# Performance work log

Measured on AMD Instinct MI355X. Metric: run time of the kernel, lower is better.

The kernel has to match this reference:

```python
import jax, jax.numpy as jnp
import numpy as np
import math

B, S, T = 32, 128, 64
FEAT = 16
H = 1024
V = 32000


def _gru_step(x, h, wih, whh, bih, bhh):
    # torch nn.GRU cell: gates ordered (r, z, n)
    gi = x @ wih.T + bih
    gh = h @ whh.T + bhh
    ir, iz, in_ = jnp.split(gi, 3, axis=-1)
    hr, hz, hn = jnp.split(gh, 3, axis=-1)
    r = jax.nn.sigmoid(ir + hr)
    z = jax.nn.sigmoid(iz + hz)
    n = jnp.tanh(in_ + r * hn)
    return (1.0 - z) * n + z * h


def _forward(features, target_tokens, temp_W, temp_b, hum_W, hum_b, cloud_W, cloud_b,
             time_W, time_b, other_W, other_b, fi_W, fi_b,
             enc_wih, enc_whh, enc_bih, enc_bhh, emb, attn_W, attn_b,
             dec_wih, dec_whh, dec_bih, dec_bhh, out_W, out_b):
    b = features.shape[0]
    # per-feature projections (dropout = identity in eval mode)
    temp = features[:, :, 0:1] @ temp_W.T + temp_b
    hum = features[:, :, 1:2] @ hum_W.T + hum_b
    cloud = features[:, :, 2:3] @ cloud_W.T + cloud_b
    time = features[:, :, -5:-3] @ time_W.T + time_b
    other_in = jnp.concatenate([features[:, :, 3:-5], features[:, :, -3:]], axis=2)
    other = other_in @ other_W.T + other_b
    concat = jnp.concatenate([temp, hum, cloud, time, other], axis=2)  # [B,S,2H]
    proj = jnp.tanh(concat @ fi_W.T + fi_b)  # [B,S,H]

    # encoder GRU over time
    def enc_step(h, x):
        h2 = _gru_step(x, h, enc_wih, enc_whh, enc_bih, enc_bhh)
        return h2, h2
    h0 = jnp.zeros((b, H), proj.dtype)
    h_last, enc_outs = jax.lax.scan(enc_step, h0, proj.transpose(1, 0, 2))
    enc_out = enc_outs.transpose(1, 0, 2)  # [B,S,H]

    # attention keys computed once (loop-invariant in the original)
    keys = enc_out @ attn_W.T + attn_b  # [B,S,H]
    scale = 1.0 / math.sqrt(H)

    # decoder: teacher_forcing_ratio = 1.0 -> input at step t is target_tokens[:, t-1]
    def dec_step(h, tok):
        e = emb[tok]  # [B,H]
        scores = jnp.einsum('bh,bsh->bs', h, keys) * scale
        w = jax.nn.softmax(scores, axis=-1)
        ctx = jnp.einsum('bs,bsh->bh', w, enc_out)
        x = jnp.concatenate([e, ctx], axis=-1)  # [B,2H]
        h2 = _gru_step(x, h, dec_wih, dec_whh, dec_bih, dec_bhh)
        pred = jnp.concatenate([h2, ctx], axis=-1) @ out_W.T + out_b  # [B,V]
        return h2, pred

    _, preds = jax.lax.scan(dec_step, h_last, target_tokens[:, :-1].T)  # [T-1,B,V]
    outputs = jnp.zeros((b, target_tokens.shape[1], V), preds.dtype)
    outputs = outputs.at[:, 0, target_tokens[0, 0]].set(1.0)
    outputs = outputs.at[:, 1:, :].set(preds.transpose(1, 0, 2))
    return outputs


def setup_inputs() -> dict:
    key = jax.random.key(0)
    ks = jax.random.split(key, 32)
    nrm = lambda k, sh: jax.random.normal(k, sh, jnp.float32) * 0.05
    Hq = H // 4
    d = {}
    d['features'] = jax.random.normal(ks[0], (B, S, FEAT), jnp.float32)
    d['target_tokens'] = jax.random.randint(ks[1], (B, T), 0, V, dtype=jnp.int32)
    d['temp_W'] = nrm(ks[2], (Hq, 1)); d['temp_b'] = nrm(ks[3], (Hq,))
    d['hum_W'] = nrm(ks[4], (Hq, 1)); d['hum_b'] = nrm(ks[5], (Hq,))
    d['cloud_W'] = nrm(ks[6], (Hq, 1)); d['cloud_b'] = nrm(ks[7], (Hq,))
    d['time_W'] = nrm(ks[8], (Hq, 2)); d['time_b'] = nrm(ks[9], (Hq,))
    d['other_W'] = nrm(ks[10], (H, FEAT - 5)); d['other_b'] = nrm(ks[11], (H,))
    d['fi_W'] = nrm(ks[12], (H, 2 * H)); d['fi_b'] = nrm(ks[13], (H,))
    d['enc_wih'] = nrm(ks[14], (3 * H, H)); d['enc_whh'] = nrm(ks[15], (3 * H, H))
    d['enc_bih'] = nrm(ks[16], (3 * H,)); d['enc_bhh'] = nrm(ks[17], (3 * H,))
    d['emb'] = nrm(ks[18], (V, H))
    d['attn_W'] = nrm(ks[19], (H, H)); d['attn_b'] = nrm(ks[20], (H,))
    d['dec_wih'] = nrm(ks[21], (3 * H, 2 * H)); d['dec_whh'] = nrm(ks[22], (3 * H, H))
    d['dec_bih'] = nrm(ks[23], (3 * H,)); d['dec_bhh'] = nrm(ks[24], (3 * H,))
    d['out_W'] = nrm(ks[25], (V, 2 * H)); d['out_b'] = nrm(ks[26], (V,))
    return d


def reference(features, target_tokens, temp_W, temp_b, hum_W, hum_b, cloud_W, cloud_b,
              time_W, time_b, other_W, other_b, fi_W, fi_b,
              enc_wih, enc_whh, enc_bih, enc_bhh, emb, attn_W, attn_b,
              dec_wih, dec_whh, dec_bih, dec_bhh, out_W, out_b):
    return _forward(features, target_tokens, temp_W, temp_b, hum_W, hum_b, cloud_W, cloud_b,
                    time_W, time_b, other_W, other_b, fi_W, fi_b,
                    enc_wih, enc_whh, enc_bih, enc_bhh, emb, attn_W, attn_b,
                    dec_wih, dec_whh, dec_bih, dec_bhh, out_W, out_b)
```

## Files before the change

### kernel.cpp

```cpp
#include <hip/hip_runtime.h>

typedef float f32x4 __attribute__((ext_vector_type(4)));
typedef __bf16 bf16x8 __attribute__((ext_vector_type(8)));

#define DI static __device__ __forceinline__

DI unsigned short f2bf(float f) {
  unsigned u = __float_as_uint(f);
  u = (u + 0x7fffu + ((u >> 16) & 1u)) >> 16;
  return (unsigned short)u;
}
DI unsigned pk2(float lo, float hi) {
  return (unsigned)f2bf(lo) | ((unsigned)f2bf(hi) << 16);
}
DI float bflo(unsigned u) { return __uint_as_float(u << 16); }
DI float bfhi(unsigned u) { return __uint_as_float(u & 0xffff0000u); }
DI float sigm(float x) { return 1.0f / (1.0f + expf(-x)); }

DI void gl_lds16(const unsigned short* g, unsigned short* l) {
  __builtin_amdgcn_global_load_lds(
      (const __attribute__((address_space(1))) unsigned int*)g,
      (__attribute__((address_space(3))) unsigned int*)l, 16, 0, 0);
}

DI void st32_sc1(unsigned* p, unsigned v) {
  __hip_atomic_store(p, v, __ATOMIC_RELAXED, __HIP_MEMORY_SCOPE_AGENT);
}
DI void st64_sc1(unsigned long long* p, unsigned long long v) {
  __hip_atomic_store(p, v, __ATOMIC_RELAXED, __HIP_MEMORY_SCOPE_AGENT);
}
DI int ldw(const int* p) {
  return __hip_atomic_load(p, __ATOMIC_RELAXED, __HIP_MEMORY_SCOPE_AGENT);
}
DI void stw(int* p, int v) {
  __hip_atomic_store(p, v, __ATOMIC_RELAXED, __HIP_MEMORY_SCOPE_AGENT);
}
DI void waitword(const int* w, int gen) {
  while (ldw(w) < gen) __builtin_amdgcn_s_sleep(1);
  asm volatile("" ::: "memory");
}

__global__ void k_fold(const float* __restrict__ tW, const float* __restrict__ tb,
                       const float* __restrict__ hW, const float* __restrict__ hb,
                       const float* __restrict__ cW, const float* __restrict__ cb,
                       const float* __restrict__ tiW, const float* __restrict__ tib,
                       const float* __restrict__ oW, const float* __restrict__ ob,
                       const float* __restrict__ fiW, const float* __restrict__ fib,
                       float* __restrict__ M, float* __restrict__ b0v)
{
  int g = blockIdx.x * 256 + threadIdx.x;
  if (g >= 1024 * 17) return;
  int h = g / 17, f = g - h * 17;
  const float* fw = fiW + (size_t)h * 2048;
  float s = 0.f;
  if (f == 16) {
    for (int k = 0; k < 256; ++k) s += fw[k] * tb[k];
    for (int k = 0; k < 256; ++k) s += fw[256 + k] * hb[k];
    for (int k = 0; k < 256; ++k) s += fw[512 + k] * cb[k];
    for (int k = 0; k < 256; ++k) s += fw[768 + k] * tib[k];
    for (int r = 0; r < 1024; ++r) s += fw[1024 + r] * ob[r];
    b0v[h] = s + fib[h];
  } else if (f == 0) {
    for (int k = 0; k < 256; ++k) s += fw[k] * tW[k];
    M[h * 16 + 0] = s;
  } else if (f == 1) {
    for (int k = 0; k < 256; ++k) s += fw[256 + k] * hW[k];
    M[h * 16 + 1] = s;
  } else if (f == 2) {
    for (int k = 0; k < 256; ++k) s += fw[512 + k] * cW[k];
    M[h * 16 + 2] = s;
  } else if (f == 11) {
    for (int k = 0; k < 256; ++k) s += fw[768 + k] * tiW[2 * k];
    M[h * 16 + 11] = s;
  } else if (f == 12) {
    for (int k = 0; k < 256; ++k) s += fw[768 + k] * tiW[2 * k + 1];
    M[h * 16 + 12] = s;
  } else {
    int col = (f <= 10) ? (f - 3) : (f - 5);
    for (int r = 0; r < 1024; ++r) s += fw[1024 + r] * oW[r * 11 + col];
    M[h * 16 + f] = s;
  }
}

__global__ __launch_bounds__(256)
void k_proj(const float* __restrict__ feat, const float* __restrict__ M,
            const float* __restrict__ b0v, unsigned short* __restrict__ proj)
{
  __shared__ float ft[16];
  int bs = blockIdx.x;
  int h = blockIdx.y * 256 + threadIdx.x;
  if (threadIdx.x < 16) ft[threadIdx.x] = feat[bs * 16 + threadIdx.x];
  __syncthreads();
  float sum = b0v[h];
  const float* mr = M + h * 16;
#pragma unroll
  for (int f = 0; f < 16; ++f) sum += mr[f] * ft[f];
  proj[(size_t)bs * 1024 + h] = f2bf(tanhf(sum));
}

__global__ void k_conv(const float* __restrict__ s, unsigned short* __restrict__ d, int n8)
{
  for (long i = (long)blockIdx.x * 256 + threadIdx.x; i < n8; i += (long)gridDim.x * 256) {
    const float* p = s + i * 8;
    f32x4 a = *(const f32x4*)p, b = *(const f32x4*)(p + 4);
    uint4 o;
    o.x = pk2(a[0], a[1]); o.y = pk2(a[2], a[3]);
    o.z = pk2(b[0], b[1]); o.w = pk2(b[2], b[3]);
    *(uint4*)(d + i * 8) = o;
  }
}

__global__ void k_conv_str(const float* __restrict__ s, unsigned short* __restrict__ d)
{
  int r = blockIdx.x;
  int c = threadIdx.x * 4;
  f32x4 a = *(const f32x4*)(s + (size_t)r * 2048 + c);
  uint2 o; o.x = pk2(a[0], a[1]); o.y = pk2(a[2], a[3]);
  *(uint2*)(d + (size_t)r * 1024 + c) = o;
}

__global__ void k_gather_e(const int* __restrict__ toks, const float* __restrict__ emb,
                           unsigned short* __restrict__ e_bf)
{
  int row = blockIdx.x;
  int t = row >> 5, b = row & 31;
  unsigned short* dst = e_bf + (size_t)row * 1024 + threadIdx.x * 4;
  if (t < 63) {
    int tok = toks[b * 64 + t];
    f32x4 a = *(const f32x4*)(emb + (size_t)tok * 1024 + threadIdx.x * 4);
    uint2 o; o.x = pk2(a[0], a[1]); o.y = pk2(a[2], a[3]);
    *(uint2*)dst = o;
  } else {
    uint2 o; o.x = 0u; o.y = 0u;
    *(uint2*)dst = o;
  }
}

__global__ void k_onehot(const int* __restrict__ toks, float* __restrict__ out)
{
  int i = blockIdx.x * 256 + threadIdx.x;
  if (i >= 32 * 32000) return;
  int b = i / 32000, v = i - b * 32000;
  out[(size_t)b * 64 * 32000 + v] = (v == toks[0]) ? 1.0f : 0.0f;
}

template<int MODE>
__global__ __launch_bounds__(256)
void gemm_bf(const unsigned short* __restrict__ A, const unsigned short* __restrict__ B,
             const float* __restrict__ bias, float* __restrict__ Cf,
             unsigned short* __restrict__ Cb,
             int tiles_m, int K, int lda, int ldb, int ldc, int coloff)
{
  __shared__ unsigned short As[4096];
  __shared__ unsigned short Bs[4096];
  const int nblk = gridDim.x;
  const int cpx = nblk >> 3;
  const int bid = blockIdx.x;
  const int id = (bid & 7) * cpx + (bid >> 3);
  const int tm = id % tiles_m, tn = id / tiles_m;
  const int tid = threadIdx.x;
  const int lane = tid & 63, wave = tid >> 6;
  const int wm = (wave & 1) << 6, wn = (wave >> 1) << 6;
  const int r0 = tid >> 2, kc0 = (tid & 3) << 3;
  const unsigned short* ga0 = A + (size_t)(tm * 128 + r0) * lda + kc0;
  const unsigned short* ga1 = A + (size_t)(tm * 128 + 64 + r0) * lda + kc0;
  const unsigned short* gb0 = B + (size_t)(tn * 128 + r0) * ldb + kc0;
  const unsigned short* gb1 = B + (size_t)(tn * 128 + 64 + r0) * ldb + kc0;
  const int lr = lane & 15, lkb = (lane >> 4) << 3;

  f32x4 acc[4][4];
#pragma unroll
  for (int m = 0; m < 4; ++m)
#pragma unroll
    for (int n = 0; n < 4; ++n) { acc[m][n][0]=0.f; acc[m][n][1]=0.f; acc[m][n][2]=0.f; acc[m][n][3]=0.f; }

  for (int kt = 0; kt < K; kt += 32) {
    __syncthreads();
    gl_lds16(ga0 + kt, &As[tid * 8]);
    gl_lds16(ga1 + kt, &As[(tid + 256) * 8]);
    gl_lds16(gb0 + kt, &Bs[tid * 8]);
    gl_lds16(gb1 + kt, &Bs[(tid + 256) * 8]);
    __syncthreads();
    bf16x8 af[4], bfv[4];
#pragma unroll
    for (int m = 0; m < 4; ++m) af[m] = *(const bf16x8*)&As[(wm + m * 16 + lr) * 32 + lkb];
#pragma unroll
    for (int n = 0; n < 4; ++n) bfv[n] = *(const bf16x8*)&Bs[(wn + n * 16 + lr) * 32 + lkb];
#pragma unroll
    for (int m = 0; m < 4; ++m)
#pragma unroll
      for (int n = 0; n < 4; ++n)
        acc[m][n] = __builtin_amdgcn_mfma_f32_16x16x32_bf16(af[m], bfv[n], acc[m][n], 0, 0, 0);
  }

#pragma unroll
  for (int m = 0; m < 4; ++m) {
    int rb = tm * 128 + wm + m * 16 + ((lane >> 4) << 2);
#pragma unroll
    for (int n = 0; n < 4; ++n) {
      int c = tn * 128 + wn + n * 16 + lr;
      float bb = bias[c];
#pragma unroll
      for (int i = 0; i < 4; ++i) {
        float v = acc[m][n][i] + bb;
        int r = rb + i;
        if (MODE == 0) {
          Cf[(size_t)r * ldc + c] = v;
        } else if (MODE == 1) {
          Cb[(size_t)r * ldc + c] = f2bf(v);
        } else {
          if (r < 2016) {
            int t = r >> 5, b2 = r & 31;
            Cf[((size_t)b2 * 64 + t + 1) * 32000 + coloff + c] = v;
          }
        }
      }
    }
  }
}

__global__ __launch_bounds__(256, 1)
void k_enc_scan(const float* __restrict__ gi_all, const float* __restrict__ whh,
                const float* __restrict__ bhh, float* __restrict__ hfp,
                unsigned short* __restrict__ enc_bf,
                int* __restrict__ arrE, int* __restrict__ relE)
{
  const int tid = threadIdx.x;
  const int blk = blockIdx.x;
  if (blk == 64) {
    if (tid < 64) {
      for (int g = 1; g <= 128; ++g) {
        for (;;) {
          int v = ldw(&arrE[tid << 2]);
          if (__all(v >= g)) break;
          __builtin_amdgcn_s_sleep(1);
        }
        asm volatile("" ::: "memory");
        if (tid == 0) stw(relE, g);
      }
    }
    return;
  }

  __shared__ unsigned short W[48 * 1024];
  __shared__ float Cred[4 * 2 * 3 * 64 * 4];
  const int lane = tid & 63, wave = tid >> 6;
  const int j0 = blk * 16;

  for (int i = tid; i < 48 * 128; i += 256) {
    int r = i >> 7, c = i & 127;
    int gr = ((r >> 4) << 10) + j0 + (r & 15);
    const float* src = whh + ((size_t)gr << 10) + (c << 3);
    f32x4 a = *(const f32x4*)src, b = *(const f32x4*)(src + 4);
    uint4 o;
    o.x = pk2(a[0], a[1]); o.y = pk2(a[2], a[3]);
    o.z = pk2(b[0], b[1]); o.w = pk2(b[2], b[3]);
    *(uint4*)&W[(r << 10) + ((c ^ (r & 7)) << 3)] = o;
  }
  __syncthreads();

  int cb[2], cj[2], clb[2], creg[2], cm[2];
  float bh0[2], bh1[2], bh2[2];
  float hp[2] = {0.f, 0.f};
#pragma unroll
  for (int cc = 0; cc < 2; ++cc) {
    int cell = tid + (cc << 8);
    cb[cc] = cell >> 4; cj[cc] = cell & 15;
    clb[cc] = ((cb[cc] & 15) >> 2) * 16;
    creg[cc] = cb[cc] & 3; cm[cc] = cb[cc] >> 4;
    bh0[cc] = bhh[j0 + cj[cc]];
    bh1[cc] = bhh[1024 + j0 + cj[cc]];
    bh2[cc] = bhh[2048 + j0 + cj[cc]];
  }

#pragma unroll 1
  for (int s = 0; s < 128; ++s) {
    float gp[2][3];
#pragma unroll
    for (int cc = 0; cc < 2; ++cc) {
      const float* gi = gi_all + ((size_t)cb[cc] * 128 + s) * 3072 + j0 + cj[cc];
      gp[cc][0] = gi[0]; gp[cc][1] = gi[1024]; gp[cc][2] = gi[2048];
    }

    f32x4 acc[2][3];
#pragma unroll
    for (int m = 0; m < 2; ++m)
#pragma unroll
      for (int n = 0; n < 3; ++n) { acc[m][n][0]=0.f; acc[m][n][1]=0.f; acc[m][n][2]=0.f; acc[m][n][3]=0.f; }

    if (s > 0) {
      waitword(relE, s);
      const unsigned short* hr = enc_bf + (size_t)(s - 1) * 1024;
      const int k0 = wave << 8;
      bf16x8 af[2][8];
#pragma unroll
      for (int kk = 0; kk < 8; ++kk) {
        int k = k0 + kk * 32 + ((lane >> 4) << 3);
        af[0][kk] = *(const bf16x8*)(hr + (size_t)(lane & 15) * 131072 + k);
        af[1][kk] = *(const bf16x8*)(hr + (size_t)(16 + (lane & 15)) * 131072 + k);
      }
#pragma unroll
      for (int kk = 0; kk < 8; ++kk) {
        int c = ((k0 + kk * 32) >> 3) + (lane >> 4);
#pragma unroll
        for (int n = 0; n < 3; ++n) {
          int wr = n * 16 + (lane & 15);
          bf16x8 bfr = *(const bf16x8*)&W[(wr << 10) + ((c ^ (wr & 7)) << 3)];
          acc[0][n] = __builtin_amdgcn_mfma_f32_16x16x32_bf16(af[0][kk], bfr, acc[0][n], 0, 0, 0);
          acc[1][n] = __builtin_amdgcn_mfma_f32_16x16x32_bf16(af[1][kk], bfr, acc[1][n], 0, 0, 0);
        }
      }
    }
#pragma unroll
    for (int m = 0; m < 2; ++m)
#pragma unroll
      for (int n = 0; n < 3; ++n)
        *(f32x4*)&Cred[((((wave * 2 + m) * 3 + n) * 64) + lane) << 2] = acc[m][n];
    __syncthreads();

    float h2v[2];
#pragma unroll
    for (int cc = 0; cc < 2; ++cc) {
      int lj = clb[cc] + cj[cc], reg = creg[cc], m = cm[cc];
      float Cr = 0.f, Cz = 0.f, Cn = 0.f;
#pragma unroll
      for (int w = 0; w < 4; ++w) {
        Cr += Cred[((((w * 2 + m) * 3 + 0) * 64 + lj) << 2) + reg];
        Cz += Cred[((((w * 2 + m) * 3 + 1) * 64 + lj) << 2) + reg];
        Cn += Cred[((((w * 2 + m) * 3 + 2) * 64 + lj) << 2) + reg];
      }
      float r = sigm(gp[cc][0] + Cr + bh0[cc]);
      float z = sigm(gp[cc][1] + Cz + bh1[cc]);
      float n = tanhf(gp[cc][2] + r * (Cn + bh2[cc]));
      float h2 = (1.f - z) * n + z * hp[cc];
      h2v[cc] = h2; hp[cc] = h2;
    }
    if (s == 127) {
      hfp[cb[0] * 1024 + j0 + cj[0]] = h2v[0];
      hfp[cb[1] * 1024 + j0 + cj[1]] = h2v[1];
    }
    unsigned short s0 = f2bf(h2v[0]), s1 = f2bf(h2v[1]);
    unsigned o0 = (unsigned)__shfl_xor((int)(unsigned)s0, 1);
    unsigned o1 = (unsigned)__shfl_xor((int)(unsigned)s1, 1);
    if ((tid & 1) == 0) {
      int j = cj[0];
      st32_sc1((unsigned*)&enc_bf[((size_t)cb[0] * 128 + s) * 1024 + j0 + j],
               (unsigned)s0 | (o0 << 16));
      st32_sc1((unsigned*)&enc_bf[((size_t)cb[1] * 128 + s) * 1024 + j0 + j],
               (unsigned)s1 | (o1 << 16));
    }
    __syncthreads();
    if (tid == 0) stw(&arrE[blk << 2], s + 1);
  }
}

__global__ __launch_bounds__(256, 1)
void k_dec_scan(const float* __restrict__ gi_e, const float* __restrict__ whh,
                const float* __restrict__ wih, const float* __restrict__ bhh,
                const unsigned short* __restrict__ keys,
                const unsigned short* __restrict__ enc_bf,
                unsigned short* __restrict__ hcat, const float* __restrict__ hfp0,
                int* __restrict__ arrC, int* __restrict__ relC,
                int* __restrict__ arrH, int* __restrict__ relH)
{
  const int tid = threadIdx.x;
  const int blk = blockIdx.x;
  if (blk == 128) {
    if (tid < 64) {
      for (int g = 1; g <= 63; ++g) {
        for (;;) {
          int v = (tid < 32) ? ldw(&arrC[tid << 2]) : g;
          if (__all(v >= g)) break;
          __builtin_amdgcn_s_sleep(1);
        }
        asm volatile("" ::: "memory");
        if (tid == 0) stw(relC, g);
        for (;;) {
          int v0 = ldw(&arrH[(tid * 2) << 2]);
          int v1 = ldw(&arrH[(tid * 2 + 1) << 2]);
          if (__all(v0 >= g && v1 >= g)) break;
          __builtin_amdgcn_s_sleep(1);
        }
        asm volatile("" ::: "memory");
        if (tid == 0) stw(relH, g);
      }
    }
    return;
  }

  __shared__ unsigned short Wh[32 * 1024];
  __shared__ unsigned short Wx[32 * 1024];
  __shared__ float Cred[4 * 2 * 2 * 64 * 4];
  __shared__ unsigned short hsh[1024];
  __shared__ float sarr[128];
  __shared__ float earr[128];
  const int lane = tid & 63, wave = tid >> 6;
  const int j0 = blk * 8;

  for (int i = tid; i < 32 * 128; i += 256) {
    int r = i >> 7, c = i & 127;
    int off = (r << 10) + ((c ^ (r & 7)) << 3);
    uint4 oh, ox;
    oh.x = oh.y = oh.z = oh.w = 0u; ox = oh;
    if (r < 24) {
      int gr = ((r >> 3) << 10) + j0 + (r & 7);
      const float* sh = whh + ((size_t)gr << 10) + (c << 3);
      f32x4 a = *(const f32x4*)sh, b = *(const f32x4*)(sh + 4);
      oh.x = pk2(a[0], a[1]); oh.y = pk2(a[2], a[3]);
      oh.z = pk2(b[0], b[1]); oh.w = pk2(b[2], b[3]);
      const float* sx = wih + ((size_t)gr << 11) + 1024 + (c << 3);
      f32x4 e = *(const f32x4*)sx, f = *(const f32x4*)(sx + 4);
      ox.x = pk2(e[0], e[1]); ox.y = pk2(e[2], e[3]);
      ox.z = pk2(f[0], f[1]); ox.w = pk2(f[2], f[3]);
    }
    *(uint4*)&Wh[off] = oh;
    *(uint4*)&Wx[off] = ox;
  }
  __syncthreads();

  const int gb = tid >> 3, gj = tid & 7;
  const int glb = ((gb & 15) >> 2) * 16;
  const int greg = gb & 3, gm = gb >> 4;
  const float bh0 = bhh[j0 + gj];
  const float bh1 = bhh[1024 + j0 + gj];
  const float bh2 = bhh[2048 + j0 + gj];
  float hpv = hfp0[gb * 1024 + j0 + gj];

#pragma unroll 1
  for (int t = 0; t < 63; ++t) {
    const int gen = t + 1;
    const float* gie = gi_e + ((size_t)t * 32 + gb) * 3072 + j0 + gj;
    float g0 = gie[0], g1 = gie[1024], g2 = gie[2048];

    if (blk < 32) {
      if (t) waitword(relH, t);
      const int b = blk;
      const unsigned short* hsrc = (t == 0)
          ? (enc_bf + (size_t)b * 131072 + (size_t)127 * 1024)
          : (hcat + ((size_t)(t - 1) * 32 + b) * 2048);
      *(uint2*)&hsh[tid * 4] = *(const uint2*)(hsrc + tid * 4);
      __syncthreads();
      {
        int sp = tid >> 1, kh = (tid & 1) << 9;
        const unsigned short* kr = keys + ((size_t)b * 128 + sp) * 1024 + kh;
        float a = 0.f;
#pragma unroll 8
        for (int c = 0; c < 512; c += 8) {
          uint4 kv = *(const uint4*)(kr + c);
          uint4 hv = *(const uint4*)&hsh[kh + c];
          a += bflo(kv.x) * bflo(hv.x) + bfhi(kv.x) * bfhi(hv.x)
             + bflo(kv.y) * bflo(hv.y) + bfhi(kv.y) * bfhi(hv.y)
             + bflo(kv.z) * bflo(hv.z) + bfhi(kv.z) * bfhi(hv.z)
             + bflo(kv.w) * bflo(hv.w) + bfhi(kv.w) * bfhi(hv.w);
        }
        a += __shfl_xor(a, 1);
        if ((tid & 1) == 0) sarr[sp] = a * 0.03125f;
      }
      __syncthreads();
      float mx = -1e30f;
#pragma unroll 16
      for (int i2 = 0; i2 < 128; ++i2) mx = fmaxf(mx, sarr[i2]);
      if (tid < 128) earr[tid] = expf(sarr[tid] - mx);
      __syncthreads();
      float sum = 0.f;
#pragma unroll 16
      for (int i2 = 0; i2 < 128; ++i2) sum += earr[i2];
      float winv = 1.f / sum;
      f32x4 cacc; cacc[0]=0.f; cacc[1]=0.f; cacc[2]=0.f; cacc[3]=0.f;
      const unsigned short* eb = enc_bf + ((size_t)b << 17) + tid * 4;
#pragma unroll 4
      for (int s2 = 0; s2 < 128; ++s2) {
        float w = earr[s2] * winv;
        uint2 ev = *(const uint2*)(eb + ((size_t)s2 << 10));
        cacc[0] += w * bflo(ev.x); cacc[1] += w * bfhi(ev.x);
        cacc[2] += w * bflo(ev.y); cacc[3] += w * bfhi(ev.y);
      }
      unsigned long long cw = (unsigned long long)pk2(cacc[0], cacc[1])
                            | ((unsigned long long)pk2(cacc[2], cacc[3]) << 32);
      st64_sc1((unsigned long long*)(hcat + ((size_t)t * 32 + b) * 2048 + 1024 + tid * 4), cw);
      __syncthreads();
      if (tid == 0) stw(&arrC[blk << 2], gen);
    }

    const int part = wave >> 1;
    const int kh2 = (wave & 1) << 9;
    const unsigned short* abase;
    size_t astr;
    const unsigned short* Wl;
    if (part == 0) {
      if (t && blk >= 32) waitword(relH, t);
      if (t == 0) { abase = enc_bf + (size_t)127 * 1024; astr = 131072; }
      else { abase = hcat + (size_t)(t - 1) * 32 * 2048; astr = 2048; }
      Wl = Wh;
    } else {
      waitword(relC, gen);
      abase = hcat + (size_t)t * 32 * 2048 + 1024; astr = 2048;
      Wl = Wx;
    }
    f32x4 acc[2][2];
#pragma unroll
    for (int m = 0; m < 2; ++m)
#pragma unroll
      for (int n = 0; n < 2; ++n) { acc[m][n][0]=0.f; acc[m][n][1]=0.f; acc[m][n][2]=0.f; acc[m][n][3]=0.f; }
#pragma unroll
    for (int hh = 0; hh < 2; ++hh) {
      bf16x8 af[2][8];
#pragma unroll
      for (int kk = 0; kk < 8; ++kk) {
        int k = kh2 + hh * 256 + kk * 32 + ((lane >> 4) << 3);
        af[0][kk] = *(const bf16x8*)(abase + (size_t)(lane & 15) * astr + k);
        af[1][kk] = *(const bf16x8*)(abase + (size_t)(16 + (lane & 15)) * astr + k);
      }
#pragma unroll
      for (int kk = 0; kk < 8; ++kk) {
        int c = ((kh2 + hh * 256 + kk * 32) >> 3) + (lane >> 4);
#pragma unroll
        for (int n = 0; n < 2; ++n) {
          int wr = n * 16 + (lane & 15);
          bf16x8 bfr = *(const bf16x8*)&Wl[(wr << 10) + ((c ^ (wr & 7)) << 3)];
          acc[0][n] = __builtin_amdgcn_mfma_f32_16x16x32_bf16(af[0][kk], bfr, acc[0][n], 0, 0, 0);
          acc[1][n] = __builtin_amdgcn_mfma_f32_16x16x32_bf16(af[1][kk], bfr, acc[1][n], 0, 0, 0);
        }
      }
    }
#pragma unroll
    for (int m = 0; m < 2; ++m)
#pragma unroll
      for (int n = 0; n < 2; ++n)
        *(f32x4*)&Cred[((((wave * 2 + m) * 2 + n) * 64) + lane) << 2] = acc[m][n];
    __syncthreads();

    {
      float Chr = 0.f, Chz = 0.f, Chn = 0.f, Cxr = 0.f, Cxz = 0.f, Cxn = 0.f;
#pragma unroll
      for (int w = 0; w < 2; ++w) {
        Chr += Cred[((((w * 2 + gm) * 2 + 0) * 64 + glb + gj) << 2) + greg];
        Chz += Cred[((((w * 2 + gm) * 2 + 0) * 64 + glb + gj + 8) << 2) + greg];
        Chn += Cred[((((w * 2 + gm) * 2 + 1) * 64 + glb + gj) << 2) + greg];
        Cxr += Cred[(((((w + 2) * 2 + gm) * 2 + 0) * 64 + glb + gj) << 2) + greg];
        Cxz += Cred[(((((w + 2) * 2 + gm) * 2 + 0) * 64 + glb + gj + 8) << 2) + greg];
        Cxn += Cred[(((((w + 2) * 2 + gm) * 2 + 1) * 64 + glb + gj) << 2) + greg];
      }
      float r = sigm(g0 + Cxr + Chr + bh0);
      float z = sigm(g1 + Cxz + Chz + bh1);
      float n2 = tanhf(g2 + Cxn + r * (Chn + bh2));
      float h2 = (1.f - z) * n2 + z * hpv;
      hpv = h2;
      unsigned short sv = f2bf(h2);
      unsigned ov = (unsigned)__shfl_xor((int)(unsigned)sv, 1);
      if ((tid & 1) == 0) {
        unsigned pv = (unsigned)sv | (ov << 16);
        st32_sc1((unsigned*)&hcat[((size_t)t * 32 + gb) * 2048 + j0 + gj], pv);
      }
    }
    __syncthreads();
    if (tid == 0) stw(&arrH[blk << 2], gen);
  }
}

extern "C" void kernel_launch(void* const* d_in, const int* in_sizes, int n_in,
                              void* d_out, int out_size, void* d_ws, size_t ws_size,
                              hipStream_t stream)
{
  const float* features = (const float*)d_in[0];
  const int*   toks     = (const int*)d_in[1];
  const float* temp_W = (const float*)d_in[2];  const float* temp_b = (const float*)d_in[3];
  const float* hum_W  = (const float*)d_in[4];  const float* hum_b  = (const float*)d_in[5];
  const float* cloud_W= (const float*)d_in[6];  const float* cloud_b= (const float*)d_in[7];
  const float* time_W = (const float*)d_in[8];  const float* time_b = (const float*)d_in[9];
  const float* other_W= (const float*)d_in[10]; const float* other_b= (const float*)d_in[11];
  const float* fi_W   = (const float*)d_in[12]; const float* fi_b   = (const float*)d_in[13];
  const float* enc_wih= (const float*)d_in[14]; const float* enc_whh= (const float*)d_in[15];
  const float* enc_bih= (const float*)d_in[16]; const float* enc_bhh= (const float*)d_in[17];
  const float* emb    = (const float*)d_in[18];
  const float* attn_W = (const float*)d_in[19]; const float* attn_b = (const float*)d_in[20];
  const float* dec_wih= (const float*)d_in[21]; const float* dec_whh= (const float*)d_in[22];
  const float* dec_bih= (const float*)d_in[23]; const float* dec_bhh= (const float*)d_in[24];
  const float* out_W  = (const float*)d_in[25]; const float* out_b  = (const float*)d_in[26];
  float* out = (float*)d_out;
  char* ws = (char*)d_ws;

  int*            arrE    = (int*)(ws + 0);
  int*            arrH    = (int*)(ws + 1024);
  int*            arrC    = (int*)(ws + 3072);
  int*            relE    = (int*)(ws + 3584);
  int*            relC    = (int*)(ws + 3600);
  int*            relH    = (int*)(ws + 3616);
  float*          Mf      = (float*)(ws + 4096);
  float*          b0v     = (float*)(ws + 69632);
  float*          hfp     = (float*)(ws + 73728);
  unsigned short* hcat    = (unsigned short*)(ws + 466944);
  unsigned short* keys_bf = (unsigned short*)(ws + 8855552);
  unsigned short* enc_bf  = (unsigned short*)(ws + 17244160);
  float*          gi_e    = (float*)(ws + 25632768);
  float*          gi_all  = (float*)(ws + 50798592);
  unsigned short* proj_bf = (unsigned short*)(ws + 101130240);
  unsigned short* e_bf    = (unsigned short*)(ws + 109518848);
  unsigned short* wihE_bf = (unsigned short*)(ws + 113713152);
  unsigned short* attnW_bf= (unsigned short*)(ws + 120004608);
  unsigned short* wihD_bf = (unsigned short*)(ws + 122101760);
  unsigned short* outW_bf = (unsigned short*)(ws + 25632768);

  hipMemsetAsync(ws, 0, 4096, stream);
  hipMemsetAsync(ws + 466944 + (size_t)2016 * 2048 * 2, 0, 32 * 2048 * 2, stream);

  k_conv<<<1536, 256, 0, stream>>>(enc_wih, wihE_bf, 393216);
  k_conv<<<512, 256, 0, stream>>>(attn_W, attnW_bf, 131072);
  k_conv_str<<<3072, 256, 0, stream>>>(dec_wih, wihD_bf);

  k_fold<<<68, 256, 0, stream>>>(temp_W, temp_b, hum_W, hum_b, cloud_W, cloud_b,
                                 time_W, time_b, other_W, other_b, fi_W, fi_b, Mf, b0v);
  k_proj<<<dim3(4096, 4), 256, 0, stream>>>(features, Mf, b0v, proj_bf);

  gemm_bf<0><<<768, 256, 0, stream>>>(proj_bf, wihE_bf, enc_bih, gi_all, nullptr,
                                      32, 1024, 1024, 1024, 3072, 0);
  k_enc_scan<<<65, 256, 0, stream>>>(gi_all, enc_whh, enc_bhh, hfp, enc_bf, arrE, relE);

  gemm_bf<1><<<256, 256, 0, stream>>>(enc_bf, attnW_bf, attn_b, nullptr, keys_bf,
                                      32, 1024, 1024, 1024, 1024, 0);
  k_gather_e<<<2048, 256, 0, stream>>>(toks, emb, e_bf);
  gemm_bf<0><<<384, 256, 0, stream>>>(e_bf, wihD_bf, dec_bih, gi_e, nullptr,
                                      16, 1024, 1024, 1024, 3072, 0);
  k_dec_scan<<<129, 256, 0, stream>>>(gi_e, dec_whh, dec_wih, dec_bhh, keys_bf,
                                      enc_bf, hcat, hfp, arrC, relC, arrH, relH);

  k_conv<<<2048, 256, 0, stream>>>(out_W, outW_bf, 4096000);
  gemm_bf<2><<<2000, 256, 0, stream>>>(hcat, outW_bf, out_b, out, nullptr,
                                       16, 2048, 2048, 2048, 0, 0);
  k_conv<<<2048, 256, 0, stream>>>(out_W + (size_t)16000 * 2048, outW_bf, 4096000);
  gemm_bf<2><<<2000, 256, 0, stream>>>(hcat, outW_bf, out_b + 16000, out, nullptr,
                                       16, 2048, 2048, 2048, 0, 16000);
  k_onehot<<<4000, 256, 0, stream>>>(toks, out);
}
```

Measured before the change: 2.974 ms.

## Split decoder attention into dedicated blocks and replicate release flags

Moves the per-batch attention and context computation out of the GRU blocks into 32 dedicated blocks, so the 128 GRU-gate blocks no longer carry that serial work. The separate release words become one generation counter replicated across 8 padded copies, and flags are spaced to avoid cache-line sharing. Polling is now done by a single lane per wave and broadcast, which is meant to reduce contention on the barrier words. The kernel launches more blocks (161), all of which must be co-resident for the spin barriers to avoid deadlock.

```diff
diff --git a/kernel.cpp b/kernel.cpp
--- a/kernel.cpp
+++ b/kernel.cpp
@@ -35,9 +35,21 @@
 DI void stw(int* p, int v) {
   __hip_atomic_store(p, v, __ATOMIC_RELAXED, __HIP_MEMORY_SCOPE_AGENT);
 }
-DI void waitword(const int* w, int gen) {
-  while (ldw(w) < gen) __builtin_amdgcn_s_sleep(1);
+
+DI void waitrel(const int* relbase, int repl, int target) {
+  const int* w = relbase + repl * 32;
+  for (;;) {
+    int v = 0;
+    if ((threadIdx.x & 63) == 0) v = ldw(w);
+    v = __shfl(v, 0);
+    if (v >= target) break;
+    __builtin_amdgcn_s_sleep(2);
+  }
   asm volatile("" ::: "memory");
+}
+DI void strel(int* relbase, int v) {
+  int l = threadIdx.x & 63;
+  if (l < 8) stw(relbase + l * 32, v);
 }
 
 __global__ void k_fold(const float* __restrict__ tW, const float* __restrict__ tb,
@@ -231,12 +243,12 @@
     if (tid < 64) {
       for (int g = 1; g <= 128; ++g) {
         for (;;) {
-          int v = ldw(&arrE[tid << 2]);
+          int v = ldw(&arrE[tid << 4]);
           if (__all(v >= g)) break;
           __builtin_amdgcn_s_sleep(1);
         }
         asm volatile("" ::: "memory");
-        if (tid == 0) stw(relE, g);
+        strel(relE, g);
       }
     }
     return;
@@ -246,6 +258,7 @@
   __shared__ float Cred[4 * 2 * 3 * 64 * 4];
   const int lane = tid & 63, wave = tid >> 6;
   const int j0 = blk * 16;
+  const int repl = blk & 7;
 
   for (int i = tid; i < 48 * 128; i += 256) {
     int r = i >> 7, c = i & 127;
@@ -289,7 +302,7 @@
       for (int n = 0; n < 3; ++n) { acc[m][n][0]=0.f; acc[m][n][1]=0.f; acc[m][n][2]=0.f; acc[m][n][3]=0.f; }
 
     if (s > 0) {
-      waitword(relE, s);
+      waitrel(relE, repl, s);
       const unsigned short* hr = enc_bf + (size_t)(s - 1) * 1024;
       const int k0 = wave << 8;
       bf16x8 af[2][8];
@@ -350,7 +363,7 @@
                (unsigned)s1 | (o1 << 16));
     }
     __syncthreads();
-    if (tid == 0) stw(&arrE[blk << 2], s + 1);
+    if (tid == 0) stw(&arrE[blk << 4], s + 1);
   }
 }
 
@@ -360,30 +373,96 @@
                 const unsigned short* __restrict__ keys,
                 const unsigned short* __restrict__ enc_bf,
                 unsigned short* __restrict__ hcat, const float* __restrict__ hfp0,
-                int* __restrict__ arrC, int* __restrict__ relC,
-                int* __restrict__ arrH, int* __restrict__ relH)
+                int* __restrict__ arrC, int* __restrict__ arrH,
+                int* __restrict__ relD)
 {
   const int tid = threadIdx.x;
   const int blk = blockIdx.x;
-  if (blk == 128) {
+  const int repl = blk & 7;
+
+  if (blk == 160) {
     if (tid < 64) {
-      for (int g = 1; g <= 63; ++g) {
+      for (int t = 0; t < 63; ++t) {
         for (;;) {
-          int v = (tid < 32) ? ldw(&arrC[tid << 2]) : g;
-          if (__all(v >= g)) break;
+          int v = (tid < 32) ? ldw(&arrC[tid << 4]) : 0x7fffffff;
+          if (__all(v >= t + 1)) break;
           __builtin_amdgcn_s_sleep(1);
         }
         asm volatile("" ::: "memory");
-        if (tid == 0) stw(relC, g);
+        strel(relD, 2 * t + 1);
         for (;;) {
-          int v0 = ldw(&arrH[(tid * 2) << 2]);
-          int v1 = ldw(&arrH[(tid * 2 + 1) << 2]);
-          if (__all(v0 >= g && v1 >= g)) break;
+          int v0 = ldw(&arrH[(tid * 2) << 4]);
+          int v1 = ldw(&arrH[(tid * 2 + 1) << 4]);
+          if (__all(v0 >= t + 1 && v1 >= t + 1)) break;
           __builtin_amdgcn_s_sleep(1);
         }
         asm volatile("" ::: "memory");
-        if (tid == 0) stw(relH, g);
-      }
+        strel(relD, 2 * t + 2);
+      }
+    }
+    return;
+  }
+
+  if (blk < 32) {
+    __shared__ unsigned short hsh[1024];
+    __shared__ float sarr[128];
+    __shared__ float earr[128];
+    const int b = blk;
+#pragma unroll 1
+    for (int t = 0; t < 63; ++t) {
+      if (t) waitrel(relD, repl, 2 * t);
+      const unsigned short* hsrc = (t == 0)
+          ? (enc_bf + (size_t)b * 131072 + (size_t)127 * 1024)
+          : (hcat + ((size_t)(t - 1) * 32 + b) * 2048);
+      *(uint2*)&hsh[tid * 4] = *(const uint2*)(hsrc + tid * 4);
+      __syncthreads();
+      {
+        int sp = tid >> 1, kh = (tid & 1) << 9;
+        const unsigned short* kr = keys + ((size_t)b * 128 + sp) * 1024 + kh;
+        float a0 = 0.f, a1 = 0.f, a2 = 0.f, a3 = 0.f;
+#pragma unroll 8
+        for (int c = 0; c < 512; c += 8) {
+          uint4 kv = *(const uint4*)(kr + c);
+          uint4 hv = *(const uint4*)&hsh[kh + c];
+          a0 += bflo(kv.x) * bflo(hv.x) + bfhi(kv.x) * bfhi(hv.x);
+          a1 += bflo(kv.y) * bflo(hv.y) + bfhi(kv.y) * bfhi(hv.y);
+          a2 += bflo(kv.z) * bflo(hv.z) + bfhi(kv.z) * bfhi(hv.z);
+          a3 += bflo(kv.w) * bflo(hv.w) + bfhi(kv.w) * bfhi(hv.w);
+        }
+        float a = (a0 + a1) + (a2 + a3);
+        a += __shfl_xor(a, 1);
+        if ((tid & 1) == 0) sarr[sp] = a * 0.03125f;
+      }
+      __syncthreads();
+      float m0 = -1e30f, m1 = -1e30f, m2 = -1e30f, m3 = -1e30f;
+#pragma unroll 8
+      for (int i2 = 0; i2 < 128; i2 += 4) {
+        m0 = fmaxf(m0, sarr[i2]); m1 = fmaxf(m1, sarr[i2 + 1]);
+        m2 = fmaxf(m2, sarr[i2 + 2]); m3 = fmaxf(m3, sarr[i2 + 3]);
+      }
+      float mx = fmaxf(fmaxf(m0, m1), fmaxf(m2, m3));
+      if (tid < 128) earr[tid] = expf(sarr[tid] - mx);
+      __syncthreads();
+      float s0 = 0.f, s1 = 0.f, s2 = 0.f, s3 = 0.f;
+#pragma unroll 8
+      for (int i2 = 0; i2 < 128; i2 += 4) {
+        s0 += earr[i2]; s1 += earr[i2 + 1]; s2 += earr[i2 + 2]; s3 += earr[i2 + 3];
+      }
+      float winv = 1.f / ((s0 + s1) + (s2 + s3));
+      f32x4 cacc; cacc[0]=0.f; cacc[1]=0.f; cacc[2]=0.f; cacc[3]=0.f;
+      const unsigned short* eb = enc_bf + ((size_t)b << 17) + tid * 4;
+#pragma unroll 4
+      for (int s2i = 0; s2i < 128; ++s2i) {
+        float w = earr[s2i] * winv;
+        uint2 ev = *(const uint2*)(eb + ((size_t)s2i << 10));
+        cacc[0] += w * bflo(ev.x); cacc[1] += w * bfhi(ev.x);
+        cacc[2] += w * bflo(ev.y); cacc[3] += w * bfhi(ev.y);
+      }
+      unsigned long long cw = (unsigned long long)pk2(cacc[0], cacc[1])
+                            | ((unsigned long long)pk2(cacc[2], cacc[3]) << 32);
+      st64_sc1((unsigned long long*)(hcat + ((size_t)t * 32 + b) * 2048 + 1024 + tid * 4), cw);
+      __syncthreads();
+      if (tid == 0) stw(&arrC[blk << 4], t + 1);
     }
     return;
   }
@@ -391,11 +470,9 @@
   __shared__ unsigned short Wh[32 * 1024];
   __shared__ unsigned short Wx[32 * 1024];
   __shared__ float Cred[4 * 2 * 2 * 64 * 4];
-  __shared__ unsigned short hsh[1024];
-  __shared__ float sarr[128];
-  __shared__ float earr[128];
   const int lane = tid & 63, wave = tid >> 6;
-  const int j0 = blk * 8;
+  const int gblk = blk - 32;
+  const int j0 = gblk * 8;
 
   for (int i = tid; i < 32 * 128; i += 256) {
     int r = i >> 7, c = i & 127;
@@ -428,59 +505,8 @@
 
 #pragma unroll 1
   for (int t = 0; t < 63; ++t) {
-    const int gen = t + 1;
     const float* gie = gi_e + ((size_t)t * 32 + gb) * 3072 + j0 + gj;
     float g0 = gie[0], g1 = gie[1024], g2 = gie[2048];
-
-    if (blk < 32) {
-      if (t) waitword(relH, t);
-      const int b = blk;
-      const unsigned short* hsrc = (t == 0)
-          ? (enc_bf + (size_t)b * 131072 + (size_t)127 * 1024)
-          : (hcat + ((size_t)(t - 1) * 32 + b) * 2048);
-      *(uint2*)&hsh[tid * 4] = *(const uint2*)(hsrc + tid * 4);
-      __syncthreads();
-      {
-        int sp = tid >> 1, kh = (tid & 1) << 9;
-        const unsigned short* kr = keys + ((size_t)b * 128 + sp) * 1024 + kh;
-        float a = 0.f;
-#pragma unroll 8
-        for (int c = 0; c < 512; c += 8) {
-          uint4 kv = *(const uint4*)(kr + c);
-          uint4 hv = *(const uint4*)&hsh[kh + c];
-          a += bflo(kv.x) * bflo(hv.x) + bfhi(kv.x) * bfhi(hv.x)
-             + bflo(kv.y) * bflo(hv.y) + bfhi(kv.y) * bfhi(hv.y)
-             + bflo(kv.z) * bflo(hv.z) + bfhi(kv.z) * bfhi(hv.z)
-             + bflo(kv.w) * bflo(hv.w) + bfhi(kv.w) * bfhi(hv.w);
-        }
-        a += __shfl_xor(a, 1);
-        if ((tid & 1) == 0) sarr[sp] = a * 0.03125f;
-      }
-      __syncthreads();
-      float mx = -1e30f;
-#pragma unroll 16
-      for (int i2 = 0; i2 < 128; ++i2) mx = fmaxf(mx, sarr[i2]);
-      if (tid < 128) earr[tid] = expf(sarr[tid] - mx);
-      __syncthreads();
-      float sum = 0.f;
-#pragma unroll 16
-      for (int i2 = 0; i2 < 128; ++i2) sum += earr[i2];
-      float winv = 1.f / sum;
-      f32x4 cacc; cacc[0]=0.f; cacc[1]=0.f; cacc[2]=0.f; cacc[3]=0.f;
-      const unsigned short* eb = enc_bf + ((size_t)b << 17) + tid * 4;
-#pragma unroll 4
-      for (int s2 = 0; s2 < 128; ++s2) {
-        float w = earr[s2] * winv;
-        uint2 ev = *(const uint2*)(eb + ((size_t)s2 << 10));
-        cacc[0] += w * bflo(ev.x); cacc[1] += w * bfhi(ev.x);
-        cacc[2] += w * bflo(ev.y); cacc[3] += w * bfhi(ev.y);
-      }
-      unsigned long long cw = (unsigned long long)pk2(cacc[0], cacc[1])
-                            | ((unsigned long long)pk2(cacc[2], cacc[3]) << 32);
-      st64_sc1((unsigned long long*)(hcat + ((size_t)t * 32 + b) * 2048 + 1024 + tid * 4), cw);
-      __syncthreads();
-      if (tid == 0) stw(&arrC[blk << 2], gen);
-    }
 
     const int part = wave >> 1;
     const int kh2 = (wave & 1) << 9;
@@ -488,12 +514,12 @@
     size_t astr;
     const unsigned short* Wl;
     if (part == 0) {
-      if (t && blk >= 32) waitword(relH, t);
+      if (t) waitrel(relD, repl, 2 * t);
       if (t == 0) { abase = enc_bf + (size_t)127 * 1024; astr = 131072; }
       else { abase = hcat + (size_t)(t - 1) * 32 * 2048; astr = 2048; }
       Wl = Wh;
     } else {
-      waitword(relC, gen);
+      waitrel(relD, repl, 2 * t + 1);
       abase = hcat + (size_t)t * 32 * 2048 + 1024; astr = 2048;
       Wl = Wx;
     }
@@ -554,7 +580,7 @@
       }
     }
     __syncthreads();
-    if (tid == 0) stw(&arrH[blk << 2], gen);
+    if (tid == 0) stw(&arrH[gblk << 4], t + 1);
   }
 }
 
@@ -581,28 +607,27 @@
   char* ws = (char*)d_ws;
 
   int*            arrE    = (int*)(ws + 0);
-  int*            arrH    = (int*)(ws + 1024);
-  int*            arrC    = (int*)(ws + 3072);
-  int*            relE    = (int*)(ws + 3584);
-  int*            relC    = (int*)(ws + 3600);
-  int*            relH    = (int*)(ws + 3616);
-  float*          Mf      = (float*)(ws + 4096);
-  float*          b0v     = (float*)(ws + 69632);
-  float*          hfp     = (float*)(ws + 73728);
-  unsigned short* hcat    = (unsigned short*)(ws + 466944);
-  unsigned short* keys_bf = (unsigned short*)(ws + 8855552);
-  unsigned short* enc_bf  = (unsigned short*)(ws + 17244160);
-  float*          gi_e    = (float*)(ws + 25632768);
-  float*          gi_all  = (float*)(ws + 50798592);
-  unsigned short* proj_bf = (unsigned short*)(ws + 101130240);
-  unsigned short* e_bf    = (unsigned short*)(ws + 109518848);
-  unsigned short* wihE_bf = (unsigned short*)(ws + 113713152);
-  unsigned short* attnW_bf= (unsigned short*)(ws + 120004608);
-  unsigned short* wihD_bf = (unsigned short*)(ws + 122101760);
-  unsigned short* outW_bf = (unsigned short*)(ws + 25632768);
-
-  hipMemsetAsync(ws, 0, 4096, stream);
-  hipMemsetAsync(ws + 466944 + (size_t)2016 * 2048 * 2, 0, 32 * 2048 * 2, stream);
+  int*            arrH    = (int*)(ws + 4096);
+  int*            arrC    = (int*)(ws + 12288);
+  int*            relE    = (int*)(ws + 14336);
+  int*            relD    = (int*)(ws + 15360);
+  float*          Mf      = (float*)(ws + 16384);
+  float*          b0v     = (float*)(ws + 81920);
+  float*          hfp     = (float*)(ws + 86016);
+  unsigned short* hcat    = (unsigned short*)(ws + 217088);
+  unsigned short* keys_bf = (unsigned short*)(ws + 8605696);
+  unsigned short* enc_bf  = (unsigned short*)(ws + 16994304);
+  float*          gi_e    = (float*)(ws + 25382912);
+  float*          gi_all  = (float*)(ws + 50548736);
+  unsigned short* proj_bf = (unsigned short*)(ws + 100880384);
+  unsigned short* e_bf    = (unsigned short*)(ws + 109268992);
+  unsigned short* wihE_bf = (unsigned short*)(ws + 113463296);
+  unsigned short* attnW_bf= (unsigned short*)(ws + 119754752);
+  unsigned short* wihD_bf = (unsigned short*)(ws + 121851904);
+  unsigned short* outW_bf = (unsigned short*)(ws + 25382912);
+
+  hipMemsetAsync(ws, 0, 16384, stream);
+  hipMemsetAsync(ws + 217088 + (size_t)2016 * 2048 * 2, 0, 32 * 2048 * 2, stream);
 
   k_conv<<<1536, 256, 0, stream>>>(enc_wih, wihE_bf, 393216);
   k_conv<<<512, 256, 0, stream>>>(attn_W, attnW_bf, 131072);
@@ -621,8 +646,8 @@
   k_gather_e<<<2048, 256, 0, stream>>>(toks, emb, e_bf);
   gemm_bf<0><<<384, 256, 0, stream>>>(e_bf, wihD_bf, dec_bih, gi_e, nullptr,
                                       16, 1024, 1024, 1024, 3072, 0);
-  k_dec_scan<<<129, 256, 0, stream>>>(gi_e, dec_whh, dec_wih, dec_bhh, keys_bf,
-                                      enc_bf, hcat, hfp, arrC, relC, arrH, relH);
+  k_dec_scan<<<161, 256, 0, stream>>>(gi_e, dec_whh, dec_wih, dec_bhh, keys_bf,
+                                      enc_bf, hcat, hfp, arrC, arrH, relD);
 
   k_conv<<<2048, 256, 0, stream>>>(out_W, outW_bf, 4096000);
   gemm_bf<2><<<2000, 256, 0, stream>>>(hcat, outW_bf, out_b, out, nullptr,
```

Result: faster. 2.645 ms (-11.1%).
